# Kernel optimization log

Hardware: AMD Instinct MI355X
Metric: run time of the kernel (lower is better)

The kernel has to match this reference:

```python
import jax, jax.numpy as jnp
import numpy as np

D_MODEL = 1024
N_HEADS = 16
HEAD_DIM = D_MODEL // N_HEADS


def setup_inputs() -> dict:
    key = jax.random.key(0)
    ks = jax.random.split(key, 9)
    s = 1.0 / np.sqrt(D_MODEL)
    x = jax.random.normal(ks[0], (2, 2048, D_MODEL), dtype=jnp.float32)
    Wq = jax.random.uniform(ks[1], (D_MODEL, D_MODEL), jnp.float32, -s, s)
    bq = jax.random.uniform(ks[2], (D_MODEL,), jnp.float32, -s, s)
    Wk = jax.random.uniform(ks[3], (D_MODEL, D_MODEL), jnp.float32, -s, s)
    bk = jax.random.uniform(ks[4], (D_MODEL,), jnp.float32, -s, s)
    Wv = jax.random.uniform(ks[5], (D_MODEL, D_MODEL), jnp.float32, -s, s)
    bv = jax.random.uniform(ks[6], (D_MODEL,), jnp.float32, -s, s)
    Wo = jax.random.uniform(ks[7], (D_MODEL, D_MODEL), jnp.float32, -s, s)
    bo = jax.random.uniform(ks[8], (D_MODEL,), jnp.float32, -s, s)
    return {"x": x, "Wq": Wq, "bq": bq, "Wk": Wk, "bk": bk,
            "Wv": Wv, "bv": bv, "Wo": Wo, "bo": bo}


def reference(x, Wq, bq, Wk, bk, Wv, bv, Wo, bo):
    B, L, _ = x.shape
    # Linear projections (torch Linear: y = x @ W.T + b; here W stored as [in, out])
    def split_heads(t):  # [B, L, D] -> [B, H, L, hd]
        return t.reshape(B, L, N_HEADS, HEAD_DIM).transpose(0, 2, 1, 3)
    Q = split_heads(x @ Wq + bq)
    K = split_heads(x @ Wk + bk)
    V = split_heads(x @ Wv + bv)
    scores = jnp.einsum('bhqd,bhkd->bhqk', Q, K) / np.sqrt(HEAD_DIM).astype(np.float32)
    attn = jax.nn.softmax(scores, axis=-1)
    out = jnp.einsum('bhqk,bhkd->bhqd', attn, V)
    out = out.transpose(0, 2, 1, 3).reshape(B, L, D_MODEL)
    return out @ Wo + bo
```

## Files before the change

kernel.cpp:

```cpp
#include <hip/hip_runtime.h>

typedef float f32x4  __attribute__((ext_vector_type(4)));
typedef short s16x8  __attribute__((ext_vector_type(8)));
typedef short s16x4  __attribute__((ext_vector_type(4)));
typedef unsigned short u16x8 __attribute__((ext_vector_type(8)));
typedef unsigned int   u32x2 __attribute__((ext_vector_type(2)));

#define DM   1024
#define LSEQ 2048
#define NH   16
#define HD   64
#define MTOT 4096
#define RS   3072
#define NT   (LSEQ / 64)

__device__ __forceinline__ unsigned short f2bf(float f) {
  union { float f; unsigned int u; } v; v.f = f;
  unsigned int r = (v.u + 0x7fffu + ((v.u >> 16) & 1u)) >> 16;
  return (unsigned short)r;
}

__device__ __forceinline__ unsigned cvtpk(float lo, float hi) {
  unsigned r;
  asm volatile("v_cvt_pk_bf16_f32 %0, %1, %2" : "=v"(r) : "v"(lo), "v"(hi));
  return r;
}

__global__ __launch_bounds__(256) void xconv(const float* __restrict__ x,
                                             unsigned short* __restrict__ xb) {
  long i = ((long)blockIdx.x * 256 + threadIdx.x) * 8;
  float4 a = *(const float4*)&x[i];
  float4 b = *(const float4*)&x[i + 4];
  u16x8 o;
  o[0] = f2bf(a.x); o[1] = f2bf(a.y); o[2] = f2bf(a.z); o[3] = f2bf(a.w);
  o[4] = f2bf(b.x); o[5] = f2bf(b.y); o[6] = f2bf(b.z); o[7] = f2bf(b.w);
  *(u16x8*)&xb[i] = o;
}

__global__ __launch_bounds__(256) void wtrans4(const float* __restrict__ W0,
                                               const float* __restrict__ W1,
                                               const float* __restrict__ W2,
                                               const float* __restrict__ W3,
                                               unsigned short* __restrict__ Wt) {
  __shared__ __align__(16) unsigned short t[64][72];
  const int z = blockIdx.z;
  const float* W = (z == 0) ? W0 : (z == 1) ? W1 : (z == 2) ? W2 : W3;
  unsigned short* dst = Wt + (size_t)z * DM * DM;
  const int n0 = blockIdx.x * 64, k0 = blockIdx.y * 64;
  const int r = threadIdx.x >> 4, c4 = (threadIdx.x & 15) * 4;
#pragma unroll
  for (int rr = r; rr < 64; rr += 16) {
    float4 v = *(const float4*)&W[(long)(k0 + rr) * DM + n0 + c4];
    ushort4 u;
    u.x = f2bf(v.x); u.y = f2bf(v.y); u.z = f2bf(v.z); u.w = f2bf(v.w);
    *(ushort4*)&t[rr][c4] = u;
  }
  __syncthreads();
#pragma unroll
  for (int rr = r; rr < 64; rr += 16) {
    ushort4 u;
    u.x = t[c4 + 0][rr]; u.y = t[c4 + 1][rr];
    u.z = t[c4 + 2][rr]; u.w = t[c4 + 3][rr];
    *(ushort4*)&dst[(long)(n0 + rr) * DM + k0 + c4] = u;
  }
}

__global__ __launch_bounds__(256) void vtrans(const unsigned short* __restrict__ QKV,
                                              unsigned short* __restrict__ VT) {
  __shared__ __align__(16) unsigned short t[64][72];
  const int bh = blockIdx.y, st = blockIdx.x;
  const int b = bh >> 4, h = bh & 15;
  const int r = threadIdx.x >> 3, c8 = (threadIdx.x & 7) * 8;
#pragma unroll
  for (int rr = r; rr < 64; rr += 32) {
    const unsigned short* Vg = QKV + (size_t)(b * LSEQ + st * 64 + rr) * RS + 2 * DM + h * HD;
    *(u16x8*)&t[rr][c8] = *(const u16x8*)&Vg[c8];
  }
  __syncthreads();
  unsigned short* Vo = VT + (size_t)(bh * HD) * LSEQ + st * 64;
#pragma unroll
  for (int rr = r; rr < 64; rr += 32) {
    u16x8 u;
#pragma unroll
    for (int j = 0; j < 8; ++j) u[j] = t[c8 + j][rr];
    *(u16x8*)&Vo[(size_t)rr * LSEQ + c8] = u;
  }
}

template <int QKV_MODE>
__global__ __launch_bounds__(256) void gemm_bt(
    const unsigned short* __restrict__ A, const unsigned short* __restrict__ Bt,
    const float* __restrict__ bias0, const float* __restrict__ bias1,
    const float* __restrict__ bias2, void* __restrict__ Cout, int N, int K) {
  __shared__ __align__(16) unsigned short As[128][72];
  __shared__ __align__(16) unsigned short Bs[128][72];
  const int tid = threadIdx.x;
  const int lane = tid & 63, w = tid >> 6;
  const int r16 = lane & 15, g = lane >> 4;
  const int m0 = blockIdx.y * 128, n0 = blockIdx.x * 128;
  const int wm = (w >> 1) * 64, wn = (w & 1) * 64;
  const int srow = tid >> 2, scol = (tid & 3) * 8;
  const unsigned short* Ag = A + (long)(m0 + srow) * K + scol;
  const unsigned short* Bg = Bt + (long)(n0 + srow) * K + scol;
  f32x4 acc[4][4] = {};
  s16x8 a0 = *(const s16x8*)Ag;
  s16x8 a1 = *(const s16x8*)(Ag + 32);
  s16x8 a2 = *(const s16x8*)(Ag + 64L * K);
  s16x8 a3 = *(const s16x8*)(Ag + 64L * K + 32);
  s16x8 b0 = *(const s16x8*)Bg;
  s16x8 b1 = *(const s16x8*)(Bg + 32);
  s16x8 b2 = *(const s16x8*)(Bg + 64L * K);
  s16x8 b3 = *(const s16x8*)(Bg + 64L * K + 32);
  for (int kt = 0; kt < K; kt += 64) {
    __syncthreads();
    *(s16x8*)&As[srow][scol]           = a0;
    *(s16x8*)&As[srow][scol + 32]      = a1;
    *(s16x8*)&As[srow + 64][scol]      = a2;
    *(s16x8*)&As[srow + 64][scol + 32] = a3;
    *(s16x8*)&Bs[srow][scol]           = b0;
    *(s16x8*)&Bs[srow][scol + 32]      = b1;
    *(s16x8*)&Bs[srow + 64][scol]      = b2;
    *(s16x8*)&Bs[srow + 64][scol + 32] = b3;
    __syncthreads();
    if (kt + 64 < K) {
      const unsigned short* An = Ag + kt + 64;
      const unsigned short* Bn = Bg + kt + 64;
      a0 = *(const s16x8*)An;
      a1 = *(const s16x8*)(An + 32);
      a2 = *(const s16x8*)(An + 64L * K);
      a3 = *(const s16x8*)(An + 64L * K + 32);
      b0 = *(const s16x8*)Bn;
      b1 = *(const s16x8*)(Bn + 32);
      b2 = *(const s16x8*)(Bn + 64L * K);
      b3 = *(const s16x8*)(Bn + 64L * K + 32);
    }
#pragma unroll
    for (int kk = 0; kk < 64; kk += 32) {
      s16x8 af[4], bf[4];
#pragma unroll
      for (int i = 0; i < 4; i++) af[i] = *(const s16x8*)&As[wm + i * 16 + r16][kk + g * 8];
#pragma unroll
      for (int j = 0; j < 4; j++) bf[j] = *(const s16x8*)&Bs[wn + j * 16 + r16][kk + g * 8];
#pragma unroll
      for (int i = 0; i < 4; i++)
#pragma unroll
        for (int j = 0; j < 4; j++)
          acc[i][j] = __builtin_amdgcn_mfma_f32_16x16x32_bf16(af[i], bf[j], acc[i][j], 0, 0, 0);
    }
  }
#pragma unroll
  for (int i = 0; i < 4; i++) {
#pragma unroll
    for (int j = 0; j < 4; j++) {
      const int row = m0 + wm + i * 16 + g * 4;
      const int col = n0 + wn + j * 16 + r16;
      float bb, sc = 1.0f;
      if constexpr (QKV_MODE) {
        bb = (col < 1024) ? bias0[col] : (col < 2048) ? bias1[col - 1024] : bias2[col - 2048];
        if (col < 1024) sc = 0.18033688011112042f;
      } else {
        bb = bias0[col];
      }
#pragma unroll
      for (int r = 0; r < 4; r++) {
        float v = (acc[i][j][r] + bb) * sc;
        if constexpr (QKV_MODE)
          ((unsigned short*)Cout)[(long)(row + r) * N + col] = f2bf(v);
        else
          ((float*)Cout)[(long)(row + r) * N + col] = v;
      }
    }
  }
}

__global__ __launch_bounds__(256) void attn8(const unsigned short* __restrict__ QKV,
                                             const unsigned short* __restrict__ VT,
                                             unsigned short* __restrict__ O) {
  __shared__ __align__(16) unsigned short Ks[2][64][76];
  __shared__ __align__(16) unsigned short Vs[2][64][76];
  __shared__ float Lsum[4][32];
  const int tid = threadIdx.x;
  const int lane = tid & 63, w = tid >> 6;
  const int r16 = lane & 15, g = lane >> 4;
  const int qb = blockIdx.x, bh = blockIdx.y;
  const int b = bh >> 4, h = bh & 15;

  const unsigned short* QgA =
      QKV + (size_t)(b * LSEQ + qb * 128 + w * 32 + r16) * RS + h * HD;
  const unsigned short* QgB = QgA + 16 * RS;
  const s16x8 qa0 = *(const s16x8*)&QgA[g * 8];
  const s16x8 qa1 = *(const s16x8*)&QgA[32 + g * 8];
  const s16x8 qb0 = *(const s16x8*)&QgB[g * 8];
  const s16x8 qb1 = *(const s16x8*)&QgB[32 + g * 8];

  const unsigned short* Kb = QKV + (size_t)(b * LSEQ) * RS + DM + h * HD;
  const unsigned short* Vb = VT + (size_t)(bh * HD) * LSEQ;
  const int srow = tid >> 2, scol = (tid & 3) * 8;

  f32x4 oA[4] = {}, oB[4] = {};
  float psA[4] = {0.f, 0.f, 0.f, 0.f};
  float psB[4] = {0.f, 0.f, 0.f, 0.f};

  s16x8 k0 = *(const s16x8*)&Kb[(size_t)srow * RS + scol];
  s16x8 k1 = *(const s16x8*)&Kb[(size_t)srow * RS + scol + 32];
  s16x8 v0 = *(const s16x8*)&Vb[(size_t)srow * LSEQ + scol];
  s16x8 v1 = *(const s16x8*)&Vb[(size_t)srow * LSEQ + scol + 32];
  *(s16x8*)&Ks[0][srow][scol]      = k0;
  *(s16x8*)&Ks[0][srow][scol + 32] = k1;
  *(s16x8*)&Vs[0][srow][scol]      = v0;
  *(s16x8*)&Vs[0][srow][scol + 32] = v1;
  __syncthreads();

  for (int t = 0; t < NT; ++t) {
    const int cur = t & 1;
    if (t + 1 < NT) {
      const size_t ko = (size_t)((t + 1) * 64 + srow) * RS + scol;
      const size_t vo = (size_t)srow * LSEQ + (t + 1) * 64 + scol;
      k0 = *(const s16x8*)&Kb[ko];
      k1 = *(const s16x8*)&Kb[ko + 32];
      v0 = *(const s16x8*)&Vb[vo];
      v1 = *(const s16x8*)&Vb[vo + 32];
    }

    f32x4 sA[4], sB[4];
#pragma unroll
    for (int kc = 0; kc < 4; kc++) {
      s16x8 kb0 = *(const s16x8*)&Ks[cur][kc * 16 + r16][g * 8];
      s16x8 kb1 = *(const s16x8*)&Ks[cur][kc * 16 + r16][32 + g * 8];
      f32x4 zA = {}, zB = {};
      zA = __builtin_amdgcn_mfma_f32_16x16x32_bf16(kb0, qa0, zA, 0, 0, 0);
      sA[kc] = __builtin_amdgcn_mfma_f32_16x16x32_bf16(kb1, qa1, zA, 0, 0, 0);
      zB = __builtin_amdgcn_mfma_f32_16x16x32_bf16(kb0, qb0, zB, 0, 0, 0);
      sB[kc] = __builtin_amdgcn_mfma_f32_16x16x32_bf16(kb1, qb1, zB, 0, 0, 0);
    }

    s16x4 paA[4], paB[4];
#pragma unroll
    for (int kc = 0; kc < 4; kc++) {
      float a0f = exp2f(sA[kc][0]);
      float a1f = exp2f(sA[kc][1]);
      float a2f = exp2f(sA[kc][2]);
      float a3f = exp2f(sA[kc][3]);
      psA[0] += a0f; psA[1] += a1f; psA[2] += a2f; psA[3] += a3f;
      u32x2 pkA = {cvtpk(a0f, a1f), cvtpk(a2f, a3f)};
      paA[kc] = __builtin_bit_cast(s16x4, pkA);
      float b0f = exp2f(sB[kc][0]);
      float b1f = exp2f(sB[kc][1]);
      float b2f = exp2f(sB[kc][2]);
      float b3f = exp2f(sB[kc][3]);
      psB[0] += b0f; psB[1] += b1f; psB[2] += b2f; psB[3] += b3f;
      u32x2 pkB = {cvtpk(b0f, b1f), cvtpk(b2f, b3f)};
      paB[kc] = __builtin_bit_cast(s16x4, pkB);
    }

#pragma unroll
    for (int kc = 0; kc < 4; kc++)
#pragma unroll
      for (int dc = 0; dc < 4; dc++) {
        s16x4 vb = *(const s16x4*)&Vs[cur][dc * 16 + r16][kc * 16 + 4 * g];
        oA[dc] = __builtin_amdgcn_mfma_f32_16x16x16bf16_1k(paA[kc], vb, oA[dc], 0, 0, 0);
        oB[dc] = __builtin_amdgcn_mfma_f32_16x16x16bf16_1k(paB[kc], vb, oB[dc], 0, 0, 0);
      }

    if (t + 1 < NT) {
      *(s16x8*)&Ks[cur ^ 1][srow][scol]      = k0;
      *(s16x8*)&Ks[cur ^ 1][srow][scol + 32] = k1;
      *(s16x8*)&Vs[cur ^ 1][srow][scol]      = v0;
      *(s16x8*)&Vs[cur ^ 1][srow][scol + 32] = v1;
      __syncthreads();
    }
  }

  float totA = psA[0] + psA[1] + psA[2] + psA[3];
  totA += __shfl_xor(totA, 16);
  totA += __shfl_xor(totA, 32);
  float totB = psB[0] + psB[1] + psB[2] + psB[3];
  totB += __shfl_xor(totB, 16);
  totB += __shfl_xor(totB, 32);
  if (g == 0) {
    Lsum[w][r16]      = totA;
    Lsum[w][16 + r16] = totB;
  }
  __syncthreads();
  const float4 svA = *(const float4*)&Lsum[w][4 * g];
  const float4 svB = *(const float4*)&Lsum[w][16 + 4 * g];

  unsigned short* Og = O + (size_t)(b * LSEQ + qb * 128 + w * 32) * DM + h * HD;
#pragma unroll
  for (int r = 0; r < 4; r++) {
    const float invA = 1.0f / ((const float*)&svA)[r];
    const float invB = 1.0f / ((const float*)&svB)[r];
#pragma unroll
    for (int dc = 0; dc < 4; dc++) {
      Og[(size_t)(g * 4 + r) * DM + dc * 16 + r16]        = f2bf(oA[dc][r] * invA);
      Og[(size_t)(16 + g * 4 + r) * DM + dc * 16 + r16]   = f2bf(oB[dc][r] * invB);
    }
  }
}

extern "C" void kernel_launch(void* const* d_in, const int* in_sizes, int n_in,
                              void* d_out, int out_size, void* d_ws, size_t ws_size,
                              hipStream_t stream) {
  const float* x  = (const float*)d_in[0];
  const float* Wq = (const float*)d_in[1];
  const float* bq = (const float*)d_in[2];
  const float* Wk = (const float*)d_in[3];
  const float* bk = (const float*)d_in[4];
  const float* Wv = (const float*)d_in[5];
  const float* bv = (const float*)d_in[6];
  const float* Wo = (const float*)d_in[7];
  const float* bo = (const float*)d_in[8];

  unsigned short* xb   = (unsigned short*)d_ws;
  unsigned short* Wcat = xb + (size_t)MTOT * DM;
  unsigned short* Wot  = Wcat + (size_t)3 * DM * DM;
  unsigned short* QKVb = Wot + (size_t)DM * DM;
  unsigned short* Ob   = QKVb + (size_t)MTOT * 3 * DM;
  unsigned short* VTb  = xb;

  xconv<<<(MTOT * DM) / (256 * 8), 256, 0, stream>>>(x, xb);
  wtrans4<<<dim3(16, 16, 4), 256, 0, stream>>>(Wq, Wk, Wv, Wo, Wcat);

  gemm_bt<1><<<dim3(3 * DM / 128, MTOT / 128), 256, 0, stream>>>(
      xb, Wcat, bq, bk, bv, (void*)QKVb, 3 * DM, DM);
  vtrans<<<dim3(LSEQ / 64, 2 * NH), 256, 0, stream>>>(QKVb, VTb);
  attn8<<<dim3(LSEQ / 128, 2 * NH), 256, 0, stream>>>(QKVb, VTb, Ob);
  gemm_bt<0><<<dim3(DM / 128, MTOT / 128), 256, 0, stream>>>(
      Ob, Wot, bo, nullptr, nullptr, d_out, DM, DM);
}
```

Measured before the change: 146.6 us.

## Split attention KV sequence across two wave groups in 512-thread blocks

Attention blocks grow to 512 threads, with each half of the block processing half of the key/value sequence using its own double-buffered LDS tiles. Partial output accumulators and row sums from the second half are passed through reused LDS and added by the first half before normalization. This doubles the waves in flight for a grid that otherwise underfills the GPU. The cost is larger LDS use and an extra reduction with added barriers.

```diff
diff --git a/kernel.cpp b/kernel.cpp
--- a/kernel.cpp
+++ b/kernel.cpp
@@ -12,7 +12,6 @@
 #define HD   64
 #define MTOT 4096
 #define RS   3072
-#define NT   (LSEQ / 64)
 
 __device__ __forceinline__ unsigned short f2bf(float f) {
   union { float f; unsigned int u; } v; v.f = f;
@@ -173,29 +172,34 @@
   }
 }
 
-__global__ __launch_bounds__(256) void attn8(const unsigned short* __restrict__ QKV,
+__global__ __launch_bounds__(512) void attn9(const unsigned short* __restrict__ QKV,
                                              const unsigned short* __restrict__ VT,
                                              unsigned short* __restrict__ O) {
-  __shared__ __align__(16) unsigned short Ks[2][64][76];
-  __shared__ __align__(16) unsigned short Vs[2][64][76];
+  __shared__ __align__(16) unsigned short Ks[2][2][64][76];
+  __shared__ __align__(16) unsigned short Vs[2][2][64][76];
   __shared__ float Lsum[4][32];
   const int tid = threadIdx.x;
   const int lane = tid & 63, w = tid >> 6;
+  const int wq = w & 3;
+  const int hb = tid >> 8;
   const int r16 = lane & 15, g = lane >> 4;
   const int qb = blockIdx.x, bh = blockIdx.y;
   const int b = bh >> 4, h = bh & 15;
 
   const unsigned short* QgA =
-      QKV + (size_t)(b * LSEQ + qb * 128 + w * 32 + r16) * RS + h * HD;
+      QKV + (size_t)(b * LSEQ + qb * 128 + wq * 32 + r16) * RS + h * HD;
   const unsigned short* QgB = QgA + 16 * RS;
   const s16x8 qa0 = *(const s16x8*)&QgA[g * 8];
   const s16x8 qa1 = *(const s16x8*)&QgA[32 + g * 8];
   const s16x8 qb0 = *(const s16x8*)&QgB[g * 8];
   const s16x8 qb1 = *(const s16x8*)&QgB[32 + g * 8];
 
-  const unsigned short* Kb = QKV + (size_t)(b * LSEQ) * RS + DM + h * HD;
-  const unsigned short* Vb = VT + (size_t)(bh * HD) * LSEQ;
-  const int srow = tid >> 2, scol = (tid & 3) * 8;
+  const unsigned short* Kb =
+      QKV + (size_t)(b * LSEQ + hb * 1024) * RS + DM + h * HD;
+  const unsigned short* Vb =
+      VT + (size_t)(bh * HD) * LSEQ + hb * 1024;
+  const int t256 = tid & 255;
+  const int srow = t256 >> 2, scol = (t256 & 3) * 8;
 
   f32x4 oA[4] = {}, oB[4] = {};
   float psA[4] = {0.f, 0.f, 0.f, 0.f};
@@ -205,17 +209,17 @@
   s16x8 k1 = *(const s16x8*)&Kb[(size_t)srow * RS + scol + 32];
   s16x8 v0 = *(const s16x8*)&Vb[(size_t)srow * LSEQ + scol];
   s16x8 v1 = *(const s16x8*)&Vb[(size_t)srow * LSEQ + scol + 32];
-  *(s16x8*)&Ks[0][srow][scol]      = k0;
-  *(s16x8*)&Ks[0][srow][scol + 32] = k1;
-  *(s16x8*)&Vs[0][srow][scol]      = v0;
-  *(s16x8*)&Vs[0][srow][scol + 32] = v1;
-  __syncthreads();
-
-  for (int t = 0; t < NT; ++t) {
-    const int cur = t & 1;
-    if (t + 1 < NT) {
-      const size_t ko = (size_t)((t + 1) * 64 + srow) * RS + scol;
-      const size_t vo = (size_t)srow * LSEQ + (t + 1) * 64 + scol;
+  *(s16x8*)&Ks[hb][0][srow][scol]      = k0;
+  *(s16x8*)&Ks[hb][0][srow][scol + 32] = k1;
+  *(s16x8*)&Vs[hb][0][srow][scol]      = v0;
+  *(s16x8*)&Vs[hb][0][srow][scol + 32] = v1;
+  __syncthreads();
+
+  for (int tt = 0; tt < 16; ++tt) {
+    const int cur = tt & 1;
+    if (tt + 1 < 16) {
+      const size_t ko = (size_t)((tt + 1) * 64 + srow) * RS + scol;
+      const size_t vo = (size_t)srow * LSEQ + (tt + 1) * 64 + scol;
       k0 = *(const s16x8*)&Kb[ko];
       k1 = *(const s16x8*)&Kb[ko + 32];
       v0 = *(const s16x8*)&Vb[vo];
@@ -225,8 +229,8 @@
     f32x4 sA[4], sB[4];
 #pragma unroll
     for (int kc = 0; kc < 4; kc++) {
-      s16x8 kb0 = *(const s16x8*)&Ks[cur][kc * 16 + r16][g * 8];
-      s16x8 kb1 = *(const s16x8*)&Ks[cur][kc * 16 + r16][32 + g * 8];
+      s16x8 kb0 = *(const s16x8*)&Ks[hb][cur][kc * 16 + r16][g * 8];
+      s16x8 kb1 = *(const s16x8*)&Ks[hb][cur][kc * 16 + r16][32 + g * 8];
       f32x4 zA = {}, zB = {};
       zA = __builtin_amdgcn_mfma_f32_16x16x32_bf16(kb0, qa0, zA, 0, 0, 0);
       sA[kc] = __builtin_amdgcn_mfma_f32_16x16x32_bf16(kb1, qa1, zA, 0, 0, 0);
@@ -257,43 +261,69 @@
     for (int kc = 0; kc < 4; kc++)
 #pragma unroll
       for (int dc = 0; dc < 4; dc++) {
-        s16x4 vb = *(const s16x4*)&Vs[cur][dc * 16 + r16][kc * 16 + 4 * g];
+        s16x4 vb = *(const s16x4*)&Vs[hb][cur][dc * 16 + r16][kc * 16 + 4 * g];
         oA[dc] = __builtin_amdgcn_mfma_f32_16x16x16bf16_1k(paA[kc], vb, oA[dc], 0, 0, 0);
         oB[dc] = __builtin_amdgcn_mfma_f32_16x16x16bf16_1k(paB[kc], vb, oB[dc], 0, 0, 0);
       }
 
-    if (t + 1 < NT) {
-      *(s16x8*)&Ks[cur ^ 1][srow][scol]      = k0;
-      *(s16x8*)&Ks[cur ^ 1][srow][scol + 32] = k1;
-      *(s16x8*)&Vs[cur ^ 1][srow][scol]      = v0;
-      *(s16x8*)&Vs[cur ^ 1][srow][scol + 32] = v1;
+    if (tt + 1 < 16) {
+      *(s16x8*)&Ks[hb][cur ^ 1][srow][scol]      = k0;
+      *(s16x8*)&Ks[hb][cur ^ 1][srow][scol + 32] = k1;
+      *(s16x8*)&Vs[hb][cur ^ 1][srow][scol]      = v0;
+      *(s16x8*)&Vs[hb][cur ^ 1][srow][scol + 32] = v1;
       __syncthreads();
     }
   }
 
-  float totA = psA[0] + psA[1] + psA[2] + psA[3];
-  totA += __shfl_xor(totA, 16);
-  totA += __shfl_xor(totA, 32);
-  float totB = psB[0] + psB[1] + psB[2] + psB[3];
-  totB += __shfl_xor(totB, 16);
-  totB += __shfl_xor(totB, 32);
-  if (g == 0) {
-    Lsum[w][r16]      = totA;
-    Lsum[w][16 + r16] = totB;
-  }
-  __syncthreads();
-  const float4 svA = *(const float4*)&Lsum[w][4 * g];
-  const float4 svB = *(const float4*)&Lsum[w][16 + 4 * g];
-
-  unsigned short* Og = O + (size_t)(b * LSEQ + qb * 128 + w * 32) * DM + h * HD;
-#pragma unroll
-  for (int r = 0; r < 4; r++) {
-    const float invA = 1.0f / ((const float*)&svA)[r];
-    const float invB = 1.0f / ((const float*)&svB)[r];
+  __syncthreads();
+  float (*xo)[33] = reinterpret_cast<float(*)[33]>(&Ks[0][0][0][0]);
+  float (*xs)[9]  = reinterpret_cast<float(*)[9]>(&Vs[0][0][0][0]);
+  if (w >= 4) {
+    const int l = tid & 255;
 #pragma unroll
     for (int dc = 0; dc < 4; dc++) {
-      Og[(size_t)(g * 4 + r) * DM + dc * 16 + r16]        = f2bf(oA[dc][r] * invA);
-      Og[(size_t)(16 + g * 4 + r) * DM + dc * 16 + r16]   = f2bf(oB[dc][r] * invB);
+      *(f32x4*)&xo[l][4 * dc]      = oA[dc];
+      *(f32x4*)&xo[l][16 + 4 * dc] = oB[dc];
+    }
+#pragma unroll
+    for (int r = 0; r < 4; r++) { xs[l][r] = psA[r]; xs[l][4 + r] = psB[r]; }
+  }
+  __syncthreads();
+  float totA = 0.f, totB = 0.f;
+  if (w < 4) {
+    const int l = tid;
+#pragma unroll
+    for (int dc = 0; dc < 4; dc++) {
+      oA[dc] += *(const f32x4*)&xo[l][4 * dc];
+      oB[dc] += *(const f32x4*)&xo[l][16 + 4 * dc];
+    }
+#pragma unroll
+    for (int r = 0; r < 4; r++) { psA[r] += xs[l][r]; psB[r] += xs[l][4 + r]; }
+    totA = psA[0] + psA[1] + psA[2] + psA[3];
+    totA += __shfl_xor(totA, 16);
+    totA += __shfl_xor(totA, 32);
+    totB = psB[0] + psB[1] + psB[2] + psB[3];
+    totB += __shfl_xor(totB, 16);
+    totB += __shfl_xor(totB, 32);
+    if (g == 0) {
+      Lsum[wq][r16]      = totA;
+      Lsum[wq][16 + r16] = totB;
+    }
+  }
+  __syncthreads();
+  if (w < 4) {
+    const float4 svA = *(const float4*)&Lsum[wq][4 * g];
+    const float4 svB = *(const float4*)&Lsum[wq][16 + 4 * g];
+    unsigned short* Og = O + (size_t)(b * LSEQ + qb * 128 + wq * 32) * DM + h * HD;
+#pragma unroll
+    for (int r = 0; r < 4; r++) {
+      const float invA = 1.0f / ((const float*)&svA)[r];
+      const float invB = 1.0f / ((const float*)&svB)[r];
+#pragma unroll
+      for (int dc = 0; dc < 4; dc++) {
+        Og[(size_t)(g * 4 + r) * DM + dc * 16 + r16]      = f2bf(oA[dc][r] * invA);
+        Og[(size_t)(16 + g * 4 + r) * DM + dc * 16 + r16] = f2bf(oB[dc][r] * invB);
+      }
     }
   }
 }
@@ -324,7 +354,7 @@
   gemm_bt<1><<<dim3(3 * DM / 128, MTOT / 128), 256, 0, stream>>>(
       xb, Wcat, bq, bk, bv, (void*)QKVb, 3 * DM, DM);
   vtrans<<<dim3(LSEQ / 64, 2 * NH), 256, 0, stream>>>(QKVb, VTb);
-  attn8<<<dim3(LSEQ / 128, 2 * NH), 256, 0, stream>>>(QKVb, VTb, Ob);
+  attn9<<<dim3(LSEQ / 128, 2 * NH), 512, 0, stream>>>(QKVb, VTb, Ob);
   gemm_bt<0><<<dim3(DM / 128, MTOT / 128), 256, 0, stream>>>(
       Ob, Wot, bo, nullptr, nullptr, d_out, DM, DM);
 }
```

Measured after the change: 144.4 us. No clear change (-1.5%).
